# Performance work log

Hardware: AMD Instinct MI355X
Metric: run time of the kernel (lower is better)

Reference implementation:

```python
import jax, jax.numpy as jnp
import numpy as np

TEMPERATURE = 0.02  # args.temperature


def setup_inputs() -> dict:
    key = jax.random.key(0)
    bs, seq_len, n_vars = 64, 512, 8
    k_positive, k_negative = 3, 16
    B = bs * n_vars            # 512
    P, D = 64, 128             # patch_num, d_model
    k1, k2, k3 = jax.random.split(key, 3)
    similarity_matrix = jax.random.normal(k1, (B, k_positive + k_negative), dtype=jnp.float32)
    # rows [0:B] are the original batch embeddings, rows [B:] are the positives
    p_enc_out = jax.random.normal(k2, (B * (1 + k_positive), P, D), dtype=jnp.float32)
    negative_index = jax.random.randint(k3, (B, k_negative), 0, B)
    return {
        "similarity_matrix": similarity_matrix,
        "p_enc_out": p_enc_out,
        "negative_index": negative_index,
        "bs": bs,
        "seq_len": seq_len,
        "n_vars": n_vars,
        "k_positive": k_positive,
        "k_negative": k_negative,
    }


def reference(similarity_matrix, p_enc_out, negative_index, bs, seq_len, n_vars, k_positive, k_negative):
    B = bs * n_vars
    P = p_enc_out.shape[-2]
    # temperature-scaled softmax over (positives ++ negatives) similarity scores
    w = jax.nn.softmax(similarity_matrix / TEMPERATURE, axis=-1)  # [B, kp+kn]
    # positives: rows B: of p_enc_out, flattened per sample -> [B, kp, P*D]
    pos = p_enc_out[B:].reshape(B, k_positive, -1)
    # negatives: gather rows of the original batch by index -> [B, kn, P*D]
    neg = p_enc_out[:B][negative_index].reshape(B, k_negative, -1)
    # weighted aggregation: two batched matvecs, summed
    rebuild = (jnp.einsum('bk,bkd->bd', w[:, :k_positive], pos)
               + jnp.einsum('bk,bkd->bd', w[:, k_positive:], neg))  # [B, P*D]
    return rebuild.reshape(B, P, -1)
```

## Files before the change

kernel.cpp:

```cpp
#include <hip/hip_runtime.h>
#include <hip/hip_bf16.h>
#include <math.h>

#define BATCH   512
#define KP      3
#define KN      16
#define KTOT    (KP + KN)
#define PD      8192
#define INV_T   50.0f

#define SPLIT   8
#define CHUNK   (PD / SPLIT)
#define THREADS 256

typedef float f32x4 __attribute__((ext_vector_type(4)));

__global__ __launch_bounds__(THREADS)
void agg_rebuild_kernel(const float* __restrict__ sim,
                        const float* __restrict__ p_enc,
                        const int*   __restrict__ neg_idx,
                        float*       __restrict__ out) {
    const int b    = blockIdx.x / SPLIT;
    const int part = blockIdx.x % SPLIT;
    const int tid  = threadIdx.x;

    __shared__ float        s_w[KTOT];
    __shared__ const float* s_row[KTOT];

    if (tid == 0) {
        float v[KTOT];
        float m = -INFINITY;
        #pragma unroll
        for (int k = 0; k < KTOT; ++k) {
            v[k] = sim[(size_t)b * KTOT + k] * INV_T;
            m = fmaxf(m, v[k]);
        }
        float s = 0.0f;
        #pragma unroll
        for (int k = 0; k < KTOT; ++k) {
            v[k] = __expf(v[k] - m);
            s += v[k];
        }
        const float inv = 1.0f / s;
        #pragma unroll
        for (int k = 0; k < KTOT; ++k) s_w[k] = v[k] * inv;
    }

    if (tid < KTOT) {
        int row;
        if (tid < KP) row = BATCH + b * KP + tid;
        else          row = neg_idx[(size_t)b * KN + (tid - KP)];
        s_row[tid] = p_enc + (size_t)row * PD;
    }
    __syncthreads();

    const int d = part * CHUNK + tid * 4;
    f32x4 acc = {0.f, 0.f, 0.f, 0.f};

    #pragma unroll
    for (int k = 0; k < KP; ++k) {
        const float wk = s_w[k];
        const f32x4 x = __builtin_nontemporal_load(
            reinterpret_cast<const f32x4*>(s_row[k] + d));
        acc += wk * x;
    }
    #pragma unroll
    for (int k = KP; k < KTOT; ++k) {
        const float wk = s_w[k];
        const f32x4 x = *reinterpret_cast<const f32x4*>(s_row[k] + d);
        acc += wk * x;
    }

    __builtin_nontemporal_store(acc,
        reinterpret_cast<f32x4*>(out + (size_t)b * PD + d));
}

extern "C" void kernel_launch(void* const* d_in, const int* in_sizes, int n_in,
                              void* d_out, int out_size, void* d_ws, size_t ws_size,
                              hipStream_t stream) {
    const float* sim     = (const float*)d_in[0];
    const float* p_enc   = (const float*)d_in[1];
    const int*   neg_idx = (const int*)d_in[2];
    float*       out     = (float*)d_out;

    dim3 grid(BATCH * SPLIT);
    dim3 block(THREADS);
    agg_rebuild_kernel<<<grid, block, 0, stream>>>(sim, p_enc, neg_idx, out);
}
```

Measured before the change: 25.08 us.

## Stage batch column slices in LDS to serve negative gathers from shared memory

```diff
diff --git a/kernel.cpp b/kernel.cpp
--- a/kernel.cpp
+++ b/kernel.cpp
@@ -9,70 +9,81 @@
 #define PD      8192
 #define INV_T   50.0f
 
-#define SPLIT   8
-#define CHUNK   (PD / SPLIT)
-#define THREADS 256
+#define SLICE   32
+#define NBLK    (PD / SLICE)
+#define THREADS 512
+#define PASSES  (BATCH / (THREADS / 8))
 
 typedef float f32x4 __attribute__((ext_vector_type(4)));
 
+__global__ __launch_bounds__(256)
+void softmax_w_kernel(const float* __restrict__ sim, float* __restrict__ w_out) {
+    const int b = blockIdx.x * blockDim.x + threadIdx.x;
+    if (b >= BATCH) return;
+    float v[KTOT];
+    float m = -INFINITY;
+    #pragma unroll
+    for (int k = 0; k < KTOT; ++k) {
+        v[k] = sim[b * KTOT + k] * INV_T;
+        m = fmaxf(m, v[k]);
+    }
+    float s = 0.0f;
+    #pragma unroll
+    for (int k = 0; k < KTOT; ++k) {
+        v[k] = __expf(v[k] - m);
+        s += v[k];
+    }
+    const float inv = 1.0f / s;
+    #pragma unroll
+    for (int k = 0; k < KTOT; ++k) w_out[b * KTOT + k] = v[k] * inv;
+}
+
 __global__ __launch_bounds__(THREADS)
-void agg_rebuild_kernel(const float* __restrict__ sim,
-                        const float* __restrict__ p_enc,
+void agg_rebuild_kernel(const float* __restrict__ p_enc,
                         const int*   __restrict__ neg_idx,
+                        const float* __restrict__ w,
                         float*       __restrict__ out) {
-    const int b    = blockIdx.x / SPLIT;
-    const int part = blockIdx.x % SPLIT;
-    const int tid  = threadIdx.x;
+    const int j   = blockIdx.x;
+    const int tid = threadIdx.x;
 
-    __shared__ float        s_w[KTOT];
-    __shared__ const float* s_row[KTOT];
+    __shared__ float lds[BATCH][SLICE];
 
-    if (tid == 0) {
-        float v[KTOT];
-        float m = -INFINITY;
-        #pragma unroll
-        for (int k = 0; k < KTOT; ++k) {
-            v[k] = sim[(size_t)b * KTOT + k] * INV_T;
-            m = fmaxf(m, v[k]);
-        }
-        float s = 0.0f;
-        #pragma unroll
-        for (int k = 0; k < KTOT; ++k) {
-            v[k] = __expf(v[k] - m);
-            s += v[k];
-        }
-        const float inv = 1.0f / s;
-        #pragma unroll
-        for (int k = 0; k < KTOT; ++k) s_w[k] = v[k] * inv;
-    }
-
-    if (tid < KTOT) {
-        int row;
-        if (tid < KP) row = BATCH + b * KP + tid;
-        else          row = neg_idx[(size_t)b * KN + (tid - KP)];
-        s_row[tid] = p_enc + (size_t)row * PD;
+    #pragma unroll
+    for (int i = tid; i < BATCH * (SLICE / 4); i += THREADS) {
+        const int row  = i >> 3;
+        const int part = i & 7;
+        reinterpret_cast<f32x4*>(&lds[0][0])[i] =
+            *reinterpret_cast<const f32x4*>(
+                p_enc + (size_t)row * PD + j * SLICE + part * 4);
     }
     __syncthreads();
 
-    const int d = part * CHUNK + tid * 4;
-    f32x4 acc = {0.f, 0.f, 0.f, 0.f};
+    const int part = tid & 7;
+    const int sl   = tid >> 3;
+    const int dcol = j * SLICE + part * 4;
 
-    #pragma unroll
-    for (int k = 0; k < KP; ++k) {
-        const float wk = s_w[k];
-        const f32x4 x = __builtin_nontemporal_load(
-            reinterpret_cast<const f32x4*>(s_row[k] + d));
-        acc += wk * x;
+    for (int p = 0; p < PASSES; ++p) {
+        const int s = p * (THREADS / 8) + sl;
+        const float* wrow = w + s * KTOT;
+        const int*   irow = neg_idx + s * KN;
+
+        f32x4 acc = {0.f, 0.f, 0.f, 0.f};
+
+        #pragma unroll
+        for (int k = 0; k < KN; ++k) {
+            const int r = irow[k];
+            const f32x4 v = *reinterpret_cast<const f32x4*>(&lds[r][part * 4]);
+            acc += wrow[KP + k] * v;
+        }
+        #pragma unroll
+        for (int k = 0; k < KP; ++k) {
+            const f32x4 v = *reinterpret_cast<const f32x4*>(
+                p_enc + (size_t)(BATCH + s * KP + k) * PD + dcol);
+            acc += wrow[k] * v;
+        }
+
+        *reinterpret_cast<f32x4*>(out + (size_t)s * PD + dcol) = acc;
     }
-    #pragma unroll
-    for (int k = KP; k < KTOT; ++k) {
-        const float wk = s_w[k];
-        const f32x4 x = *reinterpret_cast<const f32x4*>(s_row[k] + d);
-        acc += wk * x;
-    }
-
-    __builtin_nontemporal_store(acc,
-        reinterpret_cast<f32x4*>(out + (size_t)b * PD + d));
 }
 
 extern "C" void kernel_launch(void* const* d_in, const int* in_sizes, int n_in,
@@ -82,8 +93,9 @@
     const float* p_enc   = (const float*)d_in[1];
     const int*   neg_idx = (const int*)d_in[2];
     float*       out     = (float*)d_out;
+    float*       w_ws    = (float*)d_ws;
 
-    dim3 grid(BATCH * SPLIT);
-    dim3 block(THREADS);
-    agg_rebuild_kernel<<<grid, block, 0, stream>>>(sim, p_enc, neg_idx, out);
+    softmax_w_kernel<<<dim3(2), dim3(256), 0, stream>>>(sim, w_ws);
+    agg_rebuild_kernel<<<dim3(NBLK), dim3(THREADS), 0, stream>>>(
+        p_enc, neg_idx, w_ws, out);
 }
```

Result: faster. 24.30 us (-3.1%).
